# Performance work log

Measured on AMD Instinct MI355X. Metric: run time of the kernel, lower is better.

## Reference

```python
import jax, jax.numpy as jnp
import numpy as np

N = 50000   # nodes
E = 600000  # edges
D = 128     # hidden dim
L = 3       # layers

def _gelu(x):
    return jax.nn.gelu(x, approximate=False)  # torch nn.GELU default (erf)

def setup_inputs() -> dict:
    key = jax.random.key(0)
    ks = jax.random.split(key, 20)
    s = 0.05
    return {
        "feats": jax.random.normal(ks[0], (N, D), dtype=jnp.float32),
        "edge_src": jax.random.randint(ks[1], (E,), 0, N),
        "edge_dst": jax.random.randint(ks[2], (E,), 0, N),
        "Win": jax.random.normal(ks[3], (D, D), dtype=jnp.float32) * s,
        "bin_": jnp.zeros((D,), dtype=jnp.float32),
        "Wk": jax.random.normal(ks[4], (L, D, D), dtype=jnp.float32) * s,
        "bk": jnp.zeros((L, D), dtype=jnp.float32),
        "Wq": jax.random.normal(ks[5], (L, D, D), dtype=jnp.float32) * s,
        "bq": jnp.zeros((L, D), dtype=jnp.float32),
        "Wv": jax.random.normal(ks[6], (L, D, D), dtype=jnp.float32) * s,
        "bv": jnp.zeros((L, D), dtype=jnp.float32),
        "Wl": jax.random.normal(ks[7], (L, D, D), dtype=jnp.float32) * s,
        "bl": jnp.zeros((L, D), dtype=jnp.float32),
        "Wout": jax.random.normal(ks[8], (D, 1), dtype=jnp.float32) * s,
        "bout": jnp.zeros((1,), dtype=jnp.float32),
    }

def reference(feats, edge_src, edge_dst, Win, bin_, Wk, bk, Wq, bq, Wv, bv, Wl, bl, Wout, bout):
    # input linear -> (dropout=identity) -> GELU
    h = _gelu(feats @ Win + bin_)
    # in-degree for mean aggregation (clamp to 1 to avoid div by zero)
    deg = jax.ops.segment_sum(jnp.ones((E,), h.dtype), edge_dst, num_segments=N)
    deg = jnp.maximum(deg, 1.0)[:, None]  # [N,1]
    for i in range(L):
        resid = h
        # norm='none' -> identity
        key_n = h @ Wk[i] + bk[i]    # [N,D] source transform
        qry_n = h @ Wq[i] + bq[i]    # [N,D] destination transform
        # SIRConv: per-edge message act(key[src] + query[dst]), mean over incoming edges
        msg = _gelu(key_n[edge_src] + qry_n[edge_dst])          # [E,D]
        agg = jax.ops.segment_sum(msg, edge_dst, num_segments=N) / deg  # [N,D]
        conv = agg @ Wv[i] + bv[i]
        # (dropout=identity) -> GELU -> linear -> (dropout=identity) -> residual
        h = _gelu(conv) @ Wl[i] + bl[i]
        h = h + resid
    # output norm='none' -> output linear -> squeeze(1)
    out = h @ Wout + bout  # [N,1]
    return jnp.squeeze(out, axis=1)
```

## Files before the change

### kernel.cpp

```cpp
#include <hip/hip_runtime.h>
#include <hip/hip_bf16.h>
#include <math.h>

#define NN 50000
#define EE 600000
#define DIM 128
#define LL 3
#define SCB 256
#define NBLK ((NN + SCB - 1) / SCB)
#define CTS 132

typedef float f32x16 __attribute__((ext_vector_type(16)));
typedef short bfrag __attribute__((ext_vector_type(8)));

__device__ __forceinline__ float gelu_f(float x) {
    return 0.5f * x * (1.0f + erff(x * 0.70710678118654752440f));
}

__device__ __forceinline__ ushort f2bf(float x) {
    union { float f; uint u; } v; v.f = x;
    uint r = v.u + 0x7fffu + ((v.u >> 16) & 1u);
    return (ushort)(r >> 16);
}
__device__ __forceinline__ float bf2f(ushort h) {
    union { uint u; float f; } v; v.u = ((uint)h) << 16;
    return v.f;
}

__global__ __launch_bounds__(256) void deg_kernel(const int* __restrict__ dst,
                                                  int* __restrict__ deg) {
    int e = blockIdx.x * blockDim.x + threadIdx.x;
    if (e < EE) atomicAdd(&deg[dst[e]], 1);
}

__global__ __launch_bounds__(256)
void partial_kernel(const int* __restrict__ deg, int* __restrict__ partial) {
    __shared__ int s[256];
    const int t = threadIdx.x;
    const int n = blockIdx.x * SCB + t;
    s[t] = (n < NN) ? deg[n] : 0;
    __syncthreads();
#pragma unroll
    for (int off = 128; off > 0; off >>= 1) {
        if (t < off) s[t] += s[t + off];
        __syncthreads();
    }
    if (t == 0) partial[blockIdx.x] = s[0];
}

__global__ __launch_bounds__(256)
void scanpart_kernel(const int* __restrict__ partial, int* __restrict__ pofs) {
    __shared__ int s[256];
    const int t = threadIdx.x;
    const int own = (t < NBLK) ? partial[t] : 0;
    s[t] = own;
    __syncthreads();
#pragma unroll
    for (int off = 1; off < 256; off <<= 1) {
        int v = s[t];
        int a = (t >= off) ? s[t - off] : 0;
        __syncthreads();
        s[t] = v + a;
        __syncthreads();
    }
    if (t < NBLK) pofs[t] = s[t] - own;
}

__global__ __launch_bounds__(256)
void fill_kernel(const int* __restrict__ deg, const int* __restrict__ pofs,
                 int* __restrict__ rowptr, int* __restrict__ cursor,
                 float* __restrict__ invdeg) {
    __shared__ int s[256];
    const int t = threadIdx.x;
    const int n = blockIdx.x * SCB + t;
    const int d = (n < NN) ? deg[n] : 0;
    s[t] = d;
    __syncthreads();
#pragma unroll
    for (int off = 1; off < 256; off <<= 1) {
        int v = s[t];
        int a = (t >= off) ? s[t - off] : 0;
        __syncthreads();
        s[t] = v + a;
        __syncthreads();
    }
    const int base = pofs[blockIdx.x] + s[t] - d;
    if (n < NN) {
        rowptr[n] = base;
        cursor[n] = base;
        invdeg[n] = 1.0f / (float)(d < 1 ? 1 : d);
        if (n == NN - 1) rowptr[NN] = base + d;
    }
}

__global__ __launch_bounds__(256)
void bucket_kernel(const int* __restrict__ src, const int* __restrict__ dst,
                   int* __restrict__ cursor, int* __restrict__ ebuf) {
    int e = blockIdx.x * blockDim.x + threadIdx.x;
    if (e < EE) {
        int slot = atomicAdd(&cursor[dst[e]], 1);
        ebuf[slot] = src[e];
    }
}

__global__ __launch_bounds__(256)
void wsplit_kernel(const float* __restrict__ Win, const float* __restrict__ Wk,
                   const float* __restrict__ Wq, const float* __restrict__ Wv,
                   const float* __restrict__ Wl, ushort* __restrict__ pre) {
    const int b = blockIdx.x;
    const int m = b >> 1, c = b & 1;
    const float* W;
    if (m == 0) W = Win;
    else if (m <= 3) W = Wk + (size_t)(m - 1) * DIM * DIM;
    else if (m <= 6) W = Wq + (size_t)(m - 4) * DIM * DIM;
    else if (m <= 9) W = Wv + (size_t)(m - 7) * DIM * DIM;
    else W = Wl + (size_t)(m - 10) * DIM * DIM;
    ushort* dst = pre + (size_t)m * (4 * 1024 * 8) + (size_t)c * (2 * 1024 * 8);

    const int t = threadIdx.x;
    const int kc0 = c * 64;
    const int n = t & 127, kh = t >> 7;
    const int cf = n >> 5;
#pragma unroll
    for (int g = 0; g < 4; ++g) {
        const int kl0 = kh * 32 + g * 8;
#pragma unroll
        for (int j = 0; j < 8; ++j) {
            float x = W[(size_t)(kc0 + kl0 + j) * DIM + n];
            ushort hb = f2bf(x);
            float r = x - bf2f(hb);
            const int ks = kl0 >> 4, half = (kl0 >> 3) & 1;
            const int slot = (ks * 4 + cf) * 64 + (n & 31) + 32 * half;
            dst[slot * 8 + j] = hb;
            dst[1024 * 8 + slot * 8 + j] = f2bf(r);
        }
    }
}

__global__ __launch_bounds__(256)
void agg_kernel(const float* __restrict__ key, const float* qry,
                const int* __restrict__ rowptr, const int* __restrict__ ebuf,
                const float* __restrict__ invdeg, float* agg) {
    int tid = blockIdx.x * blockDim.x + threadIdx.x;
    int n = tid >> 6;
    if (n >= NN) return;
    int c = (tid & 63) << 1;
    const float2 q2 = *(const float2*)(qry + (size_t)n * DIM + c);
    float ax = 0.f, ay = 0.f;
    int j = rowptr[n];
    const int hi = rowptr[n + 1];
    for (; j + 4 <= hi; j += 4) {
        const int s0 = ebuf[j], s1 = ebuf[j + 1], s2 = ebuf[j + 2], s3 = ebuf[j + 3];
        const float2 k0 = *(const float2*)(key + (size_t)s0 * DIM + c);
        const float2 k1 = *(const float2*)(key + (size_t)s1 * DIM + c);
        const float2 k2 = *(const float2*)(key + (size_t)s2 * DIM + c);
        const float2 k3 = *(const float2*)(key + (size_t)s3 * DIM + c);
        ax += gelu_f(k0.x + q2.x); ay += gelu_f(k0.y + q2.y);
        ax += gelu_f(k1.x + q2.x); ay += gelu_f(k1.y + q2.y);
        ax += gelu_f(k2.x + q2.x); ay += gelu_f(k2.y + q2.y);
        ax += gelu_f(k3.x + q2.x); ay += gelu_f(k3.y + q2.y);
    }
    for (; j < hi; ++j) {
        const int s = ebuf[j];
        const float2 k2 = *(const float2*)(key + (size_t)s * DIM + c);
        ax += gelu_f(k2.x + q2.x);
        ay += gelu_f(k2.y + q2.y);
    }
    const float inv = invdeg[n];
    *(float2*)(agg + (size_t)n * DIM + c) = make_float2(ax * inv, ay * inv);
}

enum { EPI_NONE = 0, EPI_GELU = 1, EPI_RESID = 2 };

__device__ __forceinline__ void stage_A(const float* __restrict__ A, int M,
                                        int row0, int kc0, int t,
                                        ushort* Ah, ushort* Al) {
    const int row = t >> 2, ks = t & 3;
    const int grow = row0 + row;
    float f[16];
    if (grow < M) {
        const float* p = A + (size_t)grow * DIM + kc0 + ks * 16;
        float4 q0 = *(const float4*)(p + 0);
        float4 q1 = *(const float4*)(p + 4);
        float4 q2 = *(const float4*)(p + 8);
        float4 q3 = *(const float4*)(p + 12);
        f[0]=q0.x; f[1]=q0.y; f[2]=q0.z; f[3]=q0.w;
        f[4]=q1.x; f[5]=q1.y; f[6]=q1.z; f[7]=q1.w;
        f[8]=q2.x; f[9]=q2.y; f[10]=q2.z; f[11]=q2.w;
        f[12]=q3.x; f[13]=q3.y; f[14]=q3.z; f[15]=q3.w;
    } else {
#pragma unroll
        for (int i = 0; i < 16; ++i) f[i] = 0.f;
    }
#pragma unroll
    for (int h = 0; h < 2; ++h) {
        bfrag hv, lv;
#pragma unroll
        for (int j = 0; j < 8; ++j) {
            float x = f[h * 8 + j];
            ushort hb = f2bf(x);
            float r = x - bf2f(hb);
            hv[j] = (short)hb;
            lv[j] = (short)f2bf(r);
        }
        const int slot = (ks * 2 + (row >> 5)) * 64 + (row & 31) + 32 * h;
        *(bfrag*)&Ah[slot * 8] = hv;
        *(bfrag*)&Al[slot * 8] = lv;
    }
}

__device__ __forceinline__ void stage_W(const ushort* __restrict__ wpre, int c,
                                        int t, ushort* Wh, ushort* Wl) {
    const float4* gh = (const float4*)(wpre + ((size_t)c * 2 + 0) * 1024 * 8);
    const float4* gl = (const float4*)(wpre + ((size_t)c * 2 + 1) * 1024 * 8);
    float4* sh = (float4*)Wh;
    float4* sl = (float4*)Wl;
#pragma unroll
    for (int i = 0; i < 4; ++i) {
        sh[i * 256 + t] = gh[i * 256 + t];
        sl[i * 256 + t] = gl[i * 256 + t];
    }
}

template <int EPI>
__device__ __forceinline__ void epilogue(float* Ct, const f32x16& acc0,
                                         const f32x16& acc1, int t, int rblk,
                                         int ch, int l, int row0,
                                         const float* __restrict__ bias,
                                         const float* __restrict__ resid,
                                         float* __restrict__ C, int M) {
    __syncthreads();
    {
        const int colbase = ch * 64 + (l & 31);
        const int rb = rblk * 32 + 4 * (l >> 5);
#pragma unroll
        for (int cf2 = 0; cf2 < 2; ++cf2) {
            const int col = colbase + cf2 * 32;
#pragma unroll
            for (int r = 0; r < 16; ++r) {
                const int rl = rb + (r & 3) + 8 * (r >> 2);
                Ct[rl * CTS + col] = (cf2 == 0 ? acc0[r] : acc1[r]);
            }
        }
    }
    __syncthreads();
    {
        const int rl = t >> 2, j = t & 3;
        const int grow = row0 + rl;
        if (grow < M) {
            float* cp = C + (size_t)grow * DIM;
            const float* rp = (EPI == EPI_RESID) ? resid + (size_t)grow * DIM : nullptr;
#pragma unroll
            for (int i = 0; i < 8; ++i) {
                const int c0 = (j + 4 * i) * 4;
                float4 v = *(const float4*)&Ct[rl * CTS + c0];
                const float4 b4 = *(const float4*)&bias[c0];
                v.x += b4.x; v.y += b4.y; v.z += b4.z; v.w += b4.w;
                if (EPI == EPI_GELU) {
                    v.x = gelu_f(v.x); v.y = gelu_f(v.y);
                    v.z = gelu_f(v.z); v.w = gelu_f(v.w);
                }
                if (EPI == EPI_RESID) {
                    const float4 r4 = *(const float4*)&rp[c0];
                    v.x += r4.x; v.y += r4.y; v.z += r4.z; v.w += r4.w;
                }
                *(float4*)&cp[c0] = v;
            }
        }
    }
    __syncthreads();
}

template <int EPI>
__global__ __launch_bounds__(256)
void gemm_mfma(const float* __restrict__ A, const ushort* __restrict__ wpre,
               const float* __restrict__ bias, const float* __restrict__ resid,
               float* __restrict__ C, int M) {
    __shared__ char smem[49152];
    ushort* Ah = (ushort*)smem;
    ushort* Al = (ushort*)(smem + 8192);
    ushort* Wh = (ushort*)(smem + 16384);
    ushort* Wl = (ushort*)(smem + 32768);
    float* Ct = (float*)smem;

    const int t = threadIdx.x;
    const int row0 = blockIdx.x * 64;
    const int w = t >> 6, l = t & 63;
    const int rblk = w & 1, ch = w >> 1;

    f32x16 acc0, acc1;
#pragma unroll
    for (int i = 0; i < 16; ++i) { acc0[i] = 0.f; acc1[i] = 0.f; }

    for (int c = 0; c < 2; ++c) {
        stage_A(A, M, row0, c * 64, t, Ah, Al);
        stage_W(wpre, c, t, Wh, Wl);
        __syncthreads();
#pragma unroll
        for (int ks = 0; ks < 4; ++ks) {
            const bfrag ah = *(const bfrag*)&Ah[((ks * 2 + rblk) * 64 + l) * 8];
            const bfrag al = *(const bfrag*)&Al[((ks * 2 + rblk) * 64 + l) * 8];
#pragma unroll
            for (int q = 0; q < 2; ++q) {
                const int cf = ch * 2 + q;
                const bfrag bh = *(const bfrag*)&Wh[((ks * 4 + cf) * 64 + l) * 8];
                const bfrag bl = *(const bfrag*)&Wl[((ks * 4 + cf) * 64 + l) * 8];
                f32x16& acc = q == 0 ? acc0 : acc1;
                acc = __builtin_amdgcn_mfma_f32_32x32x16_bf16(al, bh, acc, 0, 0, 0);
                acc = __builtin_amdgcn_mfma_f32_32x32x16_bf16(ah, bl, acc, 0, 0, 0);
                acc = __builtin_amdgcn_mfma_f32_32x32x16_bf16(ah, bh, acc, 0, 0, 0);
            }
        }
        __syncthreads();
    }
    epilogue<EPI>(Ct, acc0, acc1, t, rblk, ch, l, row0, bias, resid, C, M);
}

__global__ __launch_bounds__(256)
void gemm_mfma_kq(const float* __restrict__ A, const ushort* __restrict__ wkpre,
                  const ushort* __restrict__ wqpre, const float* __restrict__ bkb,
                  const float* __restrict__ bqb, float* __restrict__ K,
                  float* __restrict__ Q, int M) {
    __shared__ char smem[81920];
    ushort* Ah  = (ushort*)smem;
    ushort* Al  = (ushort*)(smem + 8192);
    ushort* Wkh = (ushort*)(smem + 16384);
    ushort* Wkl = (ushort*)(smem + 32768);
    ushort* Wqh = (ushort*)(smem + 49152);
    ushort* Wql = (ushort*)(smem + 65536);
    float* Ct = (float*)smem;

    const int t = threadIdx.x;
    const int row0 = blockIdx.x * 64;
    const int w = t >> 6, l = t & 63;
    const int rblk = w & 1, ch = w >> 1;

    f32x16 ak0, ak1, aq0, aq1;
#pragma unroll
    for (int i = 0; i < 16; ++i) { ak0[i] = 0.f; ak1[i] = 0.f; aq0[i] = 0.f; aq1[i] = 0.f; }

    for (int c = 0; c < 2; ++c) {
        stage_A(A, M, row0, c * 64, t, Ah, Al);
        stage_W(wkpre, c, t, Wkh, Wkl);
        stage_W(wqpre, c, t, Wqh, Wql);
        __syncthreads();
#pragma unroll
        for (int ks = 0; ks < 4; ++ks) {
            const bfrag ah = *(const bfrag*)&Ah[((ks * 2 + rblk) * 64 + l) * 8];
            const bfrag al = *(const bfrag*)&Al[((ks * 2 + rblk) * 64 + l) * 8];
#pragma unroll
            for (int q = 0; q < 2; ++q) {
                const int cf = ch * 2 + q;
                const int so = ((ks * 4 + cf) * 64 + l) * 8;
                {
                    const bfrag bh = *(const bfrag*)&Wkh[so];
                    const bfrag bl = *(const bfrag*)&Wkl[so];
                    f32x16& acc = q == 0 ? ak0 : ak1;
                    acc = __builtin_amdgcn_mfma_f32_32x32x16_bf16(al, bh, acc, 0, 0, 0);
                    acc = __builtin_amdgcn_mfma_f32_32x32x16_bf16(ah, bl, acc, 0, 0, 0);
                    acc = __builtin_amdgcn_mfma_f32_32x32x16_bf16(ah, bh, acc, 0, 0, 0);
                }
                {
                    const bfrag bh = *(const bfrag*)&Wqh[so];
                    const bfrag bl = *(const bfrag*)&Wql[so];
                    f32x16& acc = q == 0 ? aq0 : aq1;
                    acc = __builtin_amdgcn_mfma_f32_32x32x16_bf16(al, bh, acc, 0, 0, 0);
                    acc = __builtin_amdgcn_mfma_f32_32x32x16_bf16(ah, bl, acc, 0, 0, 0);
                    acc = __builtin_amdgcn_mfma_f32_32x32x16_bf16(ah, bh, acc, 0, 0, 0);
                }
            }
        }
        __syncthreads();
    }
    epilogue<EPI_NONE>(Ct, ak0, ak1, t, rblk, ch, l, row0, bkb, nullptr, K, M);
    epilogue<EPI_NONE>(Ct, aq0, aq1, t, rblk, ch, l, row0, bqb, nullptr, Q, M);
}

__global__ __launch_bounds__(256)
void gemm_mfma_vl(const float* __restrict__ A, const ushort* __restrict__ wvpre,
                  const ushort* __restrict__ wlpre, const float* __restrict__ bvb,
                  const float* __restrict__ blb, const float* __restrict__ resid,
                  float* __restrict__ C, int M) {
    __shared__ char smem[49152];
    ushort* Ah = (ushort*)smem;
    ushort* Al = (ushort*)(smem + 8192);
    ushort* Wh = (ushort*)(smem + 16384);
    ushort* Wl = (ushort*)(smem + 32768);
    float* Ct = (float*)smem;

    const int t = threadIdx.x;
    const int row0 = blockIdx.x * 64;
    const int w = t >> 6, l = t & 63;
    const int rblk = w & 1, ch = w >> 1;

    f32x16 acc0, acc1;
#pragma unroll
    for (int i = 0; i < 16; ++i) { acc0[i] = 0.f; acc1[i] = 0.f; }

    for (int c = 0; c < 2; ++c) {
        stage_A(A, M, row0, c * 64, t, Ah, Al);
        stage_W(wvpre, c, t, Wh, Wl);
        __syncthreads();
#pragma unroll
        for (int ks = 0; ks < 4; ++ks) {
            const bfrag ah = *(const bfrag*)&Ah[((ks * 2 + rblk) * 64 + l) * 8];
            const bfrag al = *(const bfrag*)&Al[((ks * 2 + rblk) * 64 + l) * 8];
#pragma unroll
            for (int q = 0; q < 2; ++q) {
                const int cf = ch * 2 + q;
                const bfrag bh = *(const bfrag*)&Wh[((ks * 4 + cf) * 64 + l) * 8];
                const bfrag bl = *(const bfrag*)&Wl[((ks * 4 + cf) * 64 + l) * 8];
                f32x16& acc = q == 0 ? acc0 : acc1;
                acc = __builtin_amdgcn_mfma_f32_32x32x16_bf16(al, bh, acc, 0, 0, 0);
                acc = __builtin_amdgcn_mfma_f32_32x32x16_bf16(ah, bl, acc, 0, 0, 0);
                acc = __builtin_amdgcn_mfma_f32_32x32x16_bf16(ah, bh, acc, 0, 0, 0);
            }
        }
        __syncthreads();
    }
    {
        const int colbase = ch * 64 + (l & 31);
        const int rb = rblk * 32 + 4 * (l >> 5);
#pragma unroll
        for (int cf2 = 0; cf2 < 2; ++cf2) {
            const int col = colbase + cf2 * 32;
            const float bv = bvb[col];
#pragma unroll
            for (int r = 0; r < 16; ++r) {
                const int rl = rb + (r & 3) + 8 * (r >> 2);
                Ct[rl * CTS + col] = gelu_f((cf2 == 0 ? acc0[r] : acc1[r]) + bv);
            }
        }
    }
    __syncthreads();
    bfrag tah[2][4], tal[2][4];
    {
        const int trow = rblk * 32 + (l & 31);
        const int khalf = (l >> 5) * 8;
#pragma unroll
        for (int c = 0; c < 2; ++c)
#pragma unroll
            for (int ks = 0; ks < 4; ++ks) {
                const float* p = &Ct[trow * CTS + c * 64 + ks * 16 + khalf];
                bfrag hv, lv;
#pragma unroll
                for (int j = 0; j < 8; ++j) {
                    float x = p[j];
                    ushort hb = f2bf(x);
                    float r = x - bf2f(hb);
                    hv[j] = (short)hb;
                    lv[j] = (short)f2bf(r);
                }
                tah[c][ks] = hv;
                tal[c][ks] = lv;
            }
    }
    __syncthreads();
    f32x16 bcc0, bcc1;
#pragma unroll
    for (int i = 0; i < 16; ++i) { bcc0[i] = 0.f; bcc1[i] = 0.f; }
    for (int c = 0; c < 2; ++c) {
        stage_W(wlpre, c, t, Wh, Wl);
        __syncthreads();
#pragma unroll
        for (int ks = 0; ks < 4; ++ks) {
            const bfrag ah = tah[c][ks];
            const bfrag al = tal[c][ks];
#pragma unroll
            for (int q = 0; q < 2; ++q) {
                const int cf = ch * 2 + q;
                const bfrag bh = *(const bfrag*)&Wh[((ks * 4 + cf) * 64 + l) * 8];
                const bfrag bl = *(const bfrag*)&Wl[((ks * 4 + cf) * 64 + l) * 8];
                f32x16& acc = q == 0 ? bcc0 : bcc1;
                acc = __builtin_amdgcn_mfma_f32_32x32x16_bf16(al, bh, acc, 0, 0, 0);
                acc = __builtin_amdgcn_mfma_f32_32x32x16_bf16(ah, bl, acc, 0, 0, 0);
                acc = __builtin_amdgcn_mfma_f32_32x32x16_bf16(ah, bh, acc, 0, 0, 0);
            }
        }
        __syncthreads();
    }
    epilogue<EPI_RESID>(Ct, bcc0, bcc1, t, rblk, ch, l, row0, blb, resid, C, M);
}

__global__ __launch_bounds__(256)
void out_kernel(const float* __restrict__ h, const float* __restrict__ Wout,
                const float* __restrict__ bout, float* __restrict__ out) {
    int tid = blockIdx.x * blockDim.x + threadIdx.x;
    int n = tid >> 5;
    if (n >= NN) return;
    int lane = tid & 31;
    const float4 h4 = *(const float4*)(h + (size_t)n * DIM + lane * 4);
    const float4 w4 = *(const float4*)(Wout + lane * 4);
    float s = h4.x * w4.x + h4.y * w4.y + h4.z * w4.z + h4.w * w4.w;
#pragma unroll
    for (int off = 16; off > 0; off >>= 1) s += __shfl_down(s, off, 32);
    if (lane == 0) out[n] = s + bout[0];
}

extern "C" void kernel_launch(void* const* d_in, const int* in_sizes, int n_in,
                              void* d_out, int out_size, void* d_ws, size_t ws_size,
                              hipStream_t stream) {
    const float* feats = (const float*)d_in[0];
    const int* esrc = (const int*)d_in[1];
    const int* edst = (const int*)d_in[2];
    const float* Win = (const float*)d_in[3];
    const float* bin_ = (const float*)d_in[4];
    const float* Wk = (const float*)d_in[5];
    const float* bk = (const float*)d_in[6];
    const float* Wq = (const float*)d_in[7];
    const float* bq = (const float*)d_in[8];
    const float* Wv = (const float*)d_in[9];
    const float* bv = (const float*)d_in[10];
    const float* Wl = (const float*)d_in[11];
    const float* bl = (const float*)d_in[12];
    const float* Wout = (const float*)d_in[13];
    const float* bout = (const float*)d_in[14];

    float* ws = (float*)d_ws;
    const size_t ND = (size_t)NN * DIM;
    float* h0 = ws;
    float* h1 = ws + ND;
    float* key = ws + 2 * ND;
    float* qry = ws + 3 * ND;
    float* invdeg = ws + 4 * ND;
    int* deg = (int*)(ws + 4 * ND + NN);
    int* rowptr = deg + NN;
    int* cursor = rowptr + NN + 1;
    int* ebuf = cursor + NN;
    int* partial = ebuf + EE;
    int* pofs = partial + NBLK;
    size_t intofs = (size_t)((pofs + NBLK) - (int*)d_ws);
    intofs = (intofs + 3) & ~(size_t)3;
    ushort* pre = (ushort*)((int*)d_ws + intofs);

    dim3 b256(256);
    const int GB = (NN + 63) / 64;
    const size_t WPM = 4 * 1024 * 8;

    wsplit_kernel<<<26, b256, 0, stream>>>(Win, Wk, Wq, Wv, Wl, pre);

    hipMemsetAsync(deg, 0, NN * sizeof(int), stream);
    deg_kernel<<<(EE + 255) / 256, b256, 0, stream>>>(edst, deg);
    partial_kernel<<<NBLK, b256, 0, stream>>>(deg, partial);
    scanpart_kernel<<<1, b256, 0, stream>>>(partial, pofs);
    fill_kernel<<<NBLK, b256, 0, stream>>>(deg, pofs, rowptr, cursor, invdeg);
    bucket_kernel<<<(EE + 255) / 256, b256, 0, stream>>>(esrc, edst, cursor, ebuf);

    gemm_mfma<EPI_GELU><<<GB, b256, 0, stream>>>(feats, pre, bin_, nullptr, h0, NN);

    const float* hin = h0;
    float* hout = h1;
    for (int i = 0; i < LL; ++i) {
        const ushort* wk = pre + (size_t)(1 + i) * WPM;
        const ushort* wq = pre + (size_t)(4 + i) * WPM;
        const ushort* wv = pre + (size_t)(7 + i) * WPM;
        const ushort* wl = pre + (size_t)(10 + i) * WPM;
        const float* bki = bk + (size_t)i * DIM;
        const float* bqi = bq + (size_t)i * DIM;
        const float* bvi = bv + (size_t)i * DIM;
        const float* bli = bl + (size_t)i * DIM;

        gemm_mfma_kq<<<GB, b256, 0, stream>>>(hin, wk, wq, bki, bqi, key, qry, NN);
        agg_kernel<<<(NN * 64) / 256, b256, 0, stream>>>(key, qry, rowptr, ebuf,
                                                         invdeg, qry);
        gemm_mfma_vl<<<GB, b256, 0, stream>>>(qry, wv, wl, bvi, bli, hin, hout, NN);
        float* tmp = (float*)hin;
        hin = hout;
        hout = tmp;
    }
    out_kernel<<<(NN * 32 + 255) / 256, b256, 0, stream>>>(hin, Wout, bout,
                                                           (float*)d_out);
}
```

Baseline: 501.7 us.

## Prefetch A chunk into registers, shrink KQ smem, raise GEMM occupancy

The GEMM kernels now load the second 64-column chunk of A into registers while the first chunk's MFMAs run, which overlaps global latency with compute. The fused K/Q GEMM reuses a single weight buffer, staging Wk and Wq one after the other with extra barriers, which cuts LDS from 80KB to 48KB. Launch bounds ask for 3 blocks per CU to raise occupancy. In exchange there are more barriers, serialized weight staging and tighter register limits that may cause spills.

```diff
diff --git a/kernel.cpp b/kernel.cpp
--- a/kernel.cpp
+++ b/kernel.cpp
@@ -172,26 +172,15 @@
 
 enum { EPI_NONE = 0, EPI_GELU = 1, EPI_RESID = 2 };
 
-__device__ __forceinline__ void stage_A(const float* __restrict__ A, int M,
-                                        int row0, int kc0, int t,
-                                        ushort* Ah, ushort* Al) {
+__device__ __forceinline__ void conv_A(const float4& q0, const float4& q1,
+                                       const float4& q2, const float4& q3,
+                                       int t, ushort* Ah, ushort* Al) {
     const int row = t >> 2, ks = t & 3;
-    const int grow = row0 + row;
     float f[16];
-    if (grow < M) {
-        const float* p = A + (size_t)grow * DIM + kc0 + ks * 16;
-        float4 q0 = *(const float4*)(p + 0);
-        float4 q1 = *(const float4*)(p + 4);
-        float4 q2 = *(const float4*)(p + 8);
-        float4 q3 = *(const float4*)(p + 12);
-        f[0]=q0.x; f[1]=q0.y; f[2]=q0.z; f[3]=q0.w;
-        f[4]=q1.x; f[5]=q1.y; f[6]=q1.z; f[7]=q1.w;
-        f[8]=q2.x; f[9]=q2.y; f[10]=q2.z; f[11]=q2.w;
-        f[12]=q3.x; f[13]=q3.y; f[14]=q3.z; f[15]=q3.w;
-    } else {
-#pragma unroll
-        for (int i = 0; i < 16; ++i) f[i] = 0.f;
-    }
+    f[0]=q0.x; f[1]=q0.y; f[2]=q0.z; f[3]=q0.w;
+    f[4]=q1.x; f[5]=q1.y; f[6]=q1.z; f[7]=q1.w;
+    f[8]=q2.x; f[9]=q2.y; f[10]=q2.z; f[11]=q2.w;
+    f[12]=q3.x; f[13]=q3.y; f[14]=q3.z; f[15]=q3.w;
 #pragma unroll
     for (int h = 0; h < 2; ++h) {
         bfrag hv, lv;
@@ -220,6 +209,15 @@
         sh[i * 256 + t] = gh[i * 256 + t];
         sl[i * 256 + t] = gl[i * 256 + t];
     }
+}
+
+__device__ __forceinline__ void mma3(f32x16& acc, const bfrag& ah, const bfrag& al,
+                                     const ushort* Wh, const ushort* Wl, int so) {
+    const bfrag bh = *(const bfrag*)&Wh[so];
+    const bfrag bl = *(const bfrag*)&Wl[so];
+    acc = __builtin_amdgcn_mfma_f32_32x32x16_bf16(al, bh, acc, 0, 0, 0);
+    acc = __builtin_amdgcn_mfma_f32_32x32x16_bf16(ah, bl, acc, 0, 0, 0);
+    acc = __builtin_amdgcn_mfma_f32_32x32x16_bf16(ah, bh, acc, 0, 0, 0);
 }
 
 template <int EPI>
@@ -272,7 +270,7 @@
 }
 
 template <int EPI>
-__global__ __launch_bounds__(256)
+__global__ __launch_bounds__(256, 3)
 void gemm_mfma(const float* __restrict__ A, const ushort* __restrict__ wpre,
                const float* __restrict__ bias, const float* __restrict__ resid,
                float* __restrict__ C, int M) {
@@ -288,46 +286,48 @@
     const int w = t >> 6, l = t & 63;
     const int rblk = w & 1, ch = w >> 1;
 
+    const bool aok = (row0 + (t >> 2)) < M;
+    const float* aptr = A + (size_t)(row0 + (t >> 2)) * DIM + (t & 3) * 16;
+    float4 a0 = {0,0,0,0}, a1 = a0, a2 = a0, a3 = a0;
+    if (aok) {
+        a0 = *(const float4*)(aptr + 0);  a1 = *(const float4*)(aptr + 4);
+        a2 = *(const float4*)(aptr + 8);  a3 = *(const float4*)(aptr + 12);
+    }
+
     f32x16 acc0, acc1;
 #pragma unroll
     for (int i = 0; i < 16; ++i) { acc0[i] = 0.f; acc1[i] = 0.f; }
 
     for (int c = 0; c < 2; ++c) {
-        stage_A(A, M, row0, c * 64, t, Ah, Al);
+        conv_A(a0, a1, a2, a3, t, Ah, Al);
         stage_W(wpre, c, t, Wh, Wl);
         __syncthreads();
+        if (c == 0 && aok) {
+            a0 = *(const float4*)(aptr + 64); a1 = *(const float4*)(aptr + 68);
+            a2 = *(const float4*)(aptr + 72); a3 = *(const float4*)(aptr + 76);
+        }
 #pragma unroll
         for (int ks = 0; ks < 4; ++ks) {
             const bfrag ah = *(const bfrag*)&Ah[((ks * 2 + rblk) * 64 + l) * 8];
             const bfrag al = *(const bfrag*)&Al[((ks * 2 + rblk) * 64 + l) * 8];
-#pragma unroll
-            for (int q = 0; q < 2; ++q) {
-                const int cf = ch * 2 + q;
-                const bfrag bh = *(const bfrag*)&Wh[((ks * 4 + cf) * 64 + l) * 8];
-                const bfrag bl = *(const bfrag*)&Wl[((ks * 4 + cf) * 64 + l) * 8];
-                f32x16& acc = q == 0 ? acc0 : acc1;
-                acc = __builtin_amdgcn_mfma_f32_32x32x16_bf16(al, bh, acc, 0, 0, 0);
-                acc = __builtin_amdgcn_mfma_f32_32x32x16_bf16(ah, bl, acc, 0, 0, 0);
-                acc = __builtin_amdgcn_mfma_f32_32x32x16_bf16(ah, bh, acc, 0, 0, 0);
-            }
+            mma3(acc0, ah, al, Wh, Wl, ((ks * 4 + ch * 2 + 0) * 64 + l) * 8);
+            mma3(acc1, ah, al, Wh, Wl, ((ks * 4 + ch * 2 + 1) * 64 + l) * 8);
         }
         __syncthreads();
     }
     epilogue<EPI>(Ct, acc0, acc1, t, rblk, ch, l, row0, bias, resid, C, M);
 }
 
-__global__ __launch_bounds__(256)
+__global__ __launch_bounds__(256, 3)
 void gemm_mfma_kq(const float* __restrict__ A, const ushort* __restrict__ wkpre,
                   const ushort* __restrict__ wqpre, const float* __restrict__ bkb,
                   const float* __restrict__ bqb, float* __restrict__ K,
                   float* __restrict__ Q, int M) {
-    __shared__ char smem[81920];
-    ushort* Ah  = (ushort*)smem;
-    ushort* Al  = (ushort*)(smem + 8192);
-    ushort* Wkh = (ushort*)(smem + 16384);
-    ushort* Wkl = (ushort*)(smem + 32768);
-    ushort* Wqh = (ushort*)(smem + 49152);
-    ushort* Wql = (ushort*)(smem + 65536);
+    __shared__ char smem[49152];
+    ushort* Ah = (ushort*)smem;
+    ushort* Al = (ushort*)(smem + 8192);
+    ushort* Wh = (ushort*)(smem + 16384);
+    ushort* Wl = (ushort*)(smem + 32768);
     float* Ct = (float*)smem;
 
     const int t = threadIdx.x;
@@ -335,40 +335,42 @@
     const int w = t >> 6, l = t & 63;
     const int rblk = w & 1, ch = w >> 1;
 
+    const bool aok = (row0 + (t >> 2)) < M;
+    const float* aptr = A + (size_t)(row0 + (t >> 2)) * DIM + (t & 3) * 16;
+    float4 a0 = {0,0,0,0}, a1 = a0, a2 = a0, a3 = a0;
+    if (aok) {
+        a0 = *(const float4*)(aptr + 0);  a1 = *(const float4*)(aptr + 4);
+        a2 = *(const float4*)(aptr + 8);  a3 = *(const float4*)(aptr + 12);
+    }
+
     f32x16 ak0, ak1, aq0, aq1;
 #pragma unroll
     for (int i = 0; i < 16; ++i) { ak0[i] = 0.f; ak1[i] = 0.f; aq0[i] = 0.f; aq1[i] = 0.f; }
 
     for (int c = 0; c < 2; ++c) {
-        stage_A(A, M, row0, c * 64, t, Ah, Al);
-        stage_W(wkpre, c, t, Wkh, Wkl);
-        stage_W(wqpre, c, t, Wqh, Wql);
-        __syncthreads();
+        conv_A(a0, a1, a2, a3, t, Ah, Al);
+        stage_W(wkpre, c, t, Wh, Wl);
+        __syncthreads();
+        if (c == 0 && aok) {
+            a0 = *(const float4*)(aptr + 64); a1 = *(const float4*)(aptr + 68);
+            a2 = *(const float4*)(aptr + 72); a3 = *(const float4*)(aptr + 76);
+        }
 #pragma unroll
         for (int ks = 0; ks < 4; ++ks) {
             const bfrag ah = *(const bfrag*)&Ah[((ks * 2 + rblk) * 64 + l) * 8];
             const bfrag al = *(const bfrag*)&Al[((ks * 2 + rblk) * 64 + l) * 8];
-#pragma unroll
-            for (int q = 0; q < 2; ++q) {
-                const int cf = ch * 2 + q;
-                const int so = ((ks * 4 + cf) * 64 + l) * 8;
-                {
-                    const bfrag bh = *(const bfrag*)&Wkh[so];
-                    const bfrag bl = *(const bfrag*)&Wkl[so];
-                    f32x16& acc = q == 0 ? ak0 : ak1;
-                    acc = __builtin_amdgcn_mfma_f32_32x32x16_bf16(al, bh, acc, 0, 0, 0);
-                    acc = __builtin_amdgcn_mfma_f32_32x32x16_bf16(ah, bl, acc, 0, 0, 0);
-                    acc = __builtin_amdgcn_mfma_f32_32x32x16_bf16(ah, bh, acc, 0, 0, 0);
-                }
-                {
-                    const bfrag bh = *(const bfrag*)&Wqh[so];
-                    const bfrag bl = *(const bfrag*)&Wql[so];
-                    f32x16& acc = q == 0 ? aq0 : aq1;
-                    acc = __builtin_amdgcn_mfma_f32_32x32x16_bf16(al, bh, acc, 0, 0, 0);
-                    acc = __builtin_amdgcn_mfma_f32_32x32x16_bf16(ah, bl, acc, 0, 0, 0);
-                    acc = __builtin_amdgcn_mfma_f32_32x32x16_bf16(ah, bh, acc, 0, 0, 0);
-                }
-            }
+            mma3(ak0, ah, al, Wh, Wl, ((ks * 4 + ch * 2 + 0) * 64 + l) * 8);
+            mma3(ak1, ah, al, Wh, Wl, ((ks * 4 + ch * 2 + 1) * 64 + l) * 8);
+        }
+        __syncthreads();
+        stage_W(wqpre, c, t, Wh, Wl);
+        __syncthreads();
+#pragma unroll
+        for (int ks = 0; ks < 4; ++ks) {
+            const bfrag ah = *(const bfrag*)&Ah[((ks * 2 + rblk) * 64 + l) * 8];
+            const bfrag al = *(const bfrag*)&Al[((ks * 2 + rblk) * 64 + l) * 8];
+            mma3(aq0, ah, al, Wh, Wl, ((ks * 4 + ch * 2 + 0) * 64 + l) * 8);
+            mma3(aq1, ah, al, Wh, Wl, ((ks * 4 + ch * 2 + 1) * 64 + l) * 8);
         }
         __syncthreads();
     }
@@ -376,7 +378,7 @@
     epilogue<EPI_NONE>(Ct, aq0, aq1, t, rblk, ch, l, row0, bqb, nullptr, Q, M);
 }
 
-__global__ __launch_bounds__(256)
+__global__ __launch_bounds__(256, 3)
 void gemm_mfma_vl(const float* __restrict__ A, const ushort* __restrict__ wvpre,
                   const ushort* __restrict__ wlpre, const float* __restrict__ bvb,
                   const float* __restrict__ blb, const float* __restrict__ resid,
@@ -393,28 +395,32 @@
     const int w = t >> 6, l = t & 63;
     const int rblk = w & 1, ch = w >> 1;
 
+    const bool aok = (row0 + (t >> 2)) < M;
+    const float* aptr = A + (size_t)(row0 + (t >> 2)) * DIM + (t & 3) * 16;
+    float4 a0 = {0,0,0,0}, a1 = a0, a2 = a0, a3 = a0;
+    if (aok) {
+        a0 = *(const float4*)(aptr + 0);  a1 = *(const float4*)(aptr + 4);
+        a2 = *(const float4*)(aptr + 8);  a3 = *(const float4*)(aptr + 12);
+    }
+
     f32x16 acc0, acc1;
 #pragma unroll
     for (int i = 0; i < 16; ++i) { acc0[i] = 0.f; acc1[i] = 0.f; }
 
     for (int c = 0; c < 2; ++c) {
-        stage_A(A, M, row0, c * 64, t, Ah, Al);
+        conv_A(a0, a1, a2, a3, t, Ah, Al);
         stage_W(wvpre, c, t, Wh, Wl);
         __syncthreads();
+        if (c == 0 && aok) {
+            a0 = *(const float4*)(aptr + 64); a1 = *(const float4*)(aptr + 68);
+            a2 = *(const float4*)(aptr + 72); a3 = *(const float4*)(aptr + 76);
+        }
 #pragma unroll
         for (int ks = 0; ks < 4; ++ks) {
             const bfrag ah = *(const bfrag*)&Ah[((ks * 2 + rblk) * 64 + l) * 8];
             const bfrag al = *(const bfrag*)&Al[((ks * 2 + rblk) * 64 + l) * 8];
-#pragma unroll
-            for (int q = 0; q < 2; ++q) {
-                const int cf = ch * 2 + q;
-                const bfrag bh = *(const bfrag*)&Wh[((ks * 4 + cf) * 64 + l) * 8];
-                const bfrag bl = *(const bfrag*)&Wl[((ks * 4 + cf) * 64 + l) * 8];
-                f32x16& acc = q == 0 ? acc0 : acc1;
-                acc = __builtin_amdgcn_mfma_f32_32x32x16_bf16(al, bh, acc, 0, 0, 0);
-                acc = __builtin_amdgcn_mfma_f32_32x32x16_bf16(ah, bl, acc, 0, 0, 0);
-                acc = __builtin_amdgcn_mfma_f32_32x32x16_bf16(ah, bh, acc, 0, 0, 0);
-            }
+            mma3(acc0, ah, al, Wh, Wl, ((ks * 4 + ch * 2 + 0) * 64 + l) * 8);
+            mma3(acc1, ah, al, Wh, Wl, ((ks * 4 + ch * 2 + 1) * 64 + l) * 8);
         }
         __syncthreads();
     }
@@ -464,18 +470,8 @@
         __syncthreads();
 #pragma unroll
         for (int ks = 0; ks < 4; ++ks) {
-            const bfrag ah = tah[c][ks];
-            const bfrag al = tal[c][ks];
-#pragma unroll
-            for (int q = 0; q < 2; ++q) {
-                const int cf = ch * 2 + q;
-                const bfrag bh = *(const bfrag*)&Wh[((ks * 4 + cf) * 64 + l) * 8];
-                const bfrag bl = *(const bfrag*)&Wl[((ks * 4 + cf) * 64 + l) * 8];
-                f32x16& acc = q == 0 ? bcc0 : bcc1;
-                acc = __builtin_amdgcn_mfma_f32_32x32x16_bf16(al, bh, acc, 0, 0, 0);
-                acc = __builtin_amdgcn_mfma_f32_32x32x16_bf16(ah, bl, acc, 0, 0, 0);
-                acc = __builtin_amdgcn_mfma_f32_32x32x16_bf16(ah, bh, acc, 0, 0, 0);
-            }
+            mma3(bcc0, tah[c][ks], tal[c][ks], Wh, Wl, ((ks * 4 + ch * 2 + 0) * 64 + l) * 8);
+            mma3(bcc1, tah[c][ks], tal[c][ks], Wh, Wl, ((ks * 4 + ch * 2 + 1) * 64 + l) * 8);
         }
         __syncthreads();
     }
```

Measured after the change: 496.5 us. About the same (-1.0%).
